# Kernel optimization log

Measured on AMD Instinct MI355X. Metric: run time of the kernel, lower is better.

Reference implementation:

```python
import jax, jax.numpy as jnp
import numpy as np

N_LAYERS = 2   # number of S6 blocks
D = 512        # input_dim / d_model
N = 16         # hid_dim (SSM state size)
O = 512        # output_dim
B = 4          # batch
L = 2048       # seq_len
LN_EPS = 1e-5


def setup_inputs() -> dict:
    key = jax.random.key(0)
    ks = jax.random.split(key, 10)
    s = D ** -0.5
    inp = {
        "x": jax.random.normal(ks[0], (B, L, D), jnp.float32),
        # per-layer S6 block params (stacked over layer axis)
        "A_log": jax.random.normal(ks[1], (N_LAYERS, D, N), jnp.float32) * 0.5,
        "W_B": jax.random.normal(ks[2], (N_LAYERS, D, N), jnp.float32) * s,
        "b_B": jnp.zeros((N_LAYERS, N), jnp.float32),
        "W_C": jax.random.normal(ks[3], (N_LAYERS, D, N), jnp.float32) * s,
        "b_C": jnp.zeros((N_LAYERS, N), jnp.float32),
        "W_dt": jax.random.normal(ks[4], (N_LAYERS, D, D), jnp.float32) * s,
        "b_dt": jnp.zeros((N_LAYERS, D), jnp.float32),
        "D_skip": jnp.ones((N_LAYERS, D), jnp.float32),
        # mixing linear + layer norm per layer
        "W_mix": jax.random.normal(ks[5], (N_LAYERS, D, D), jnp.float32) * s,
        "b_mix": jnp.zeros((N_LAYERS, D), jnp.float32),
        "ln_g": jnp.ones((N_LAYERS, D), jnp.float32),
        "ln_b": jnp.zeros((N_LAYERS, D), jnp.float32),
        # final decoder
        "W_dec": jax.random.normal(ks[6], (D, O), jnp.float32) * s,
        "b_dec": jnp.zeros((O,), jnp.float32),
    }
    return inp


def _combine(e1, e2):
    # first-order linear recurrence combine: h <- a*h + u
    a1, u1 = e1
    a2, u2 = e2
    return a1 * a2, a2 * u1 + u2


def reference(x, A_log, W_B, b_B, W_C, b_C, W_dt, b_dt, D_skip,
              W_mix, b_mix, ln_g, ln_b, W_dec, b_dec):
    h_in = x  # [B, L, D]
    for i in range(N_LAYERS):
        # ---- S6 block: input-dependent B, C, dt; diagonal A ----
        A = -jnp.exp(A_log[i])                               # [D, N], negative real
        Bm = h_in @ W_B[i] + b_B[i]                          # [B, L, N]
        Cm = h_in @ W_C[i] + b_C[i]                          # [B, L, N]
        dt = jax.nn.softplus(h_in @ W_dt[i] + b_dt[i])       # [B, L, D]
        # discretize: a_t = exp(dt*A), u_t = dt * B_t * x_t
        a = jnp.exp(dt[..., None] * A)                       # [B, L, D, N]
        u = (dt * h_in)[..., None] * Bm[:, :, None, :]       # [B, L, D, N]
        # parallel scan over sequence axis (Heinsen / Blelloch style)
        _, h = jax.lax.associative_scan(_combine, (a, u), axis=1)
        y = jnp.einsum('bln,bldn->bld', Cm, h) + D_skip[i] * h_in  # [B, L, D]
        # ---- activation (torch.nn.GELU default = exact erf) ----
        y = jax.nn.gelu(y, approximate=False)
        # ---- mixing linear ----
        y = y @ W_mix[i] + b_mix[i]
        # ---- layer norm ----
        mu = jnp.mean(y, axis=-1, keepdims=True)
        var = jnp.var(y, axis=-1, keepdims=True)
        y = (y - mu) / jnp.sqrt(var + LN_EPS) * ln_g[i] + ln_b[i]
        # ---- residual ----
        h_in = h_in + y
    return h_in @ W_dec + b_dec  # [B, L, O]
```

## Files before the change

### kernel.cpp

```cpp
#include <hip/hip_runtime.h>
#include <math.h>

typedef unsigned short u16;
typedef unsigned int u32;
typedef __attribute__((ext_vector_type(8))) short short8;
typedef __attribute__((ext_vector_type(8))) _Float16 half8;
typedef __attribute__((ext_vector_type(4))) float f32x4;

#define BL 8192
#define DD 512
#define NN 16
#define NCHUNK 64
#define SCH 32
#define ZLD 640

__device__ __forceinline__ float softplus_f(float z) {
  float w = __builtin_amdgcn_exp2f(-1.4426950408889634f * fabsf(z));
  return fmaxf(z, 0.0f) + 0.69314718055994531f * __builtin_amdgcn_logf(1.0f + w);
}

__device__ __forceinline__ float gelu_erf(float y) {
  float ax = fabsf(y) * 0.70710678118654752f;
  float t  = __builtin_amdgcn_rcpf(1.0f + 0.3275911f * ax);
  float e  = __builtin_amdgcn_exp2f(-1.4426950408889634f * ax * ax);
  float p  = ((((1.061405429f * t - 1.453152027f) * t + 1.421413741f) * t
               - 0.284496736f) * t + 0.254829592f) * t;
  float er = copysignf(1.0f - p * e, y);
  return 0.5f * y * (1.0f + er);
}

#define PREP_TOT (4194304 + 655360 + 524288 + 262144 + 1280 + 16384)
__global__ __launch_bounds__(256) void prep_kernel(
    const float* __restrict__ x, const float* __restrict__ A_log,
    const float* __restrict__ W_B, const float* __restrict__ b_B,
    const float* __restrict__ W_C, const float* __restrict__ b_C,
    const float* __restrict__ W_dt, const float* __restrict__ b_dt,
    const float* __restrict__ W_mix, const float* __restrict__ W_dec,
    _Float16* __restrict__ x16, _Float16* __restrict__ Wc16,
    _Float16* __restrict__ Wm16, _Float16* __restrict__ Wd16,
    float* __restrict__ bcat, float* __restrict__ A2)
{
  int i = blockIdx.x * 256 + threadIdx.x;
  if (i >= PREP_TOT) return;
  if (i < 4194304) { x16[i] = (_Float16)x[i]; return; }
  i -= 4194304;
  if (i < 655360) {
    int l = i / 327680, r = i % 327680, n = r >> 9, k = r & 511;
    float v = 0.0f;
    if (n < 16)       v = W_B[l * 8192 + k * 16 + n];
    else if (n < 32)  v = W_C[l * 8192 + k * 16 + (n - 16)];
    else if (n < 544) v = W_dt[l * 262144 + k * 512 + (n - 32)];
    Wc16[i] = (_Float16)v;
    return;
  }
  i -= 655360;
  if (i < 524288) {
    int l = i / 262144, r = i % 262144, n = r >> 9, k = r & 511;
    Wm16[i] = (_Float16)W_mix[l * 262144 + k * 512 + n];
    return;
  }
  i -= 524288;
  if (i < 262144) {
    int n = i >> 9, k = i & 511;
    Wd16[i] = (_Float16)W_dec[k * 512 + n];
    return;
  }
  i -= 262144;
  if (i < 1280) {
    int l = i / 640, n = i % 640;
    float v = 0.0f;
    if (n < 16)       v = b_B[l * 16 + n];
    else if (n < 32)  v = b_C[l * 16 + (n - 16)];
    else if (n < 544) v = b_dt[l * 512 + (n - 32)];
    bcat[i] = v;
    return;
  }
  i -= 1280;
  A2[i] = -expf(A_log[i]) * 1.4426950408889634f;
}

template <int MODE>
__global__ __launch_bounds__(256) void gemm_f16(
    const _Float16* __restrict__ A, const _Float16* __restrict__ Bt,
    const float* __restrict__ bias, float* __restrict__ Cmat, int ldc)
{
  const int K = 512;
  int bid = blockIdx.x;
  int xcd = bid & 7;
  int rest = bid >> 3;
  int mloc = rest & 7;
  int nb = rest >> 3;
  int m0 = (xcd * 8 + mloc) * 128;
  int n0 = nb * 64;
  __shared__ __align__(16) char smem[36864];
  _Float16* As = (_Float16*)smem;
  _Float16* Bs = As + 128 * 32;
  int tid = threadIdx.x;
  int wave = tid >> 6, lane = tid & 63;
  int wm = (wave >> 1) * 64;
  int wn = (wave & 1) * 32;
  int lrow = lane & 15;
  int lk = (lane >> 4) * 8;
  f32x4 acc[4][2] = {};

  int q0 = tid, q1 = tid + 256;
  size_t offA0 = (size_t)(m0 + (q0 >> 2)) * K + (q0 & 3) * 8;
  size_t offA1 = (size_t)(m0 + (q1 >> 2)) * K + (q1 & 3) * 8;
  size_t offB  = (size_t)(n0 + (q0 >> 2)) * K + (q0 & 3) * 8;
  unsigned l0 = (unsigned)(wave * 64) * 8;
  unsigned l1 = (unsigned)(wave * 64 + 256) * 8;

  for (int k0 = 0; k0 < K; k0 += 32) {
    __builtin_amdgcn_global_load_lds(
        (const __attribute__((address_space(1))) void*)(A + offA0 + k0),
        (__attribute__((address_space(3))) void*)(&As[l0]), 16, 0, 0);
    __builtin_amdgcn_global_load_lds(
        (const __attribute__((address_space(1))) void*)(A + offA1 + k0),
        (__attribute__((address_space(3))) void*)(&As[l1]), 16, 0, 0);
    __builtin_amdgcn_global_load_lds(
        (const __attribute__((address_space(1))) void*)(Bt + offB + k0),
        (__attribute__((address_space(3))) void*)(&Bs[l0]), 16, 0, 0);
    __syncthreads();

    half8 af[4], bf[2];
#pragma unroll
    for (int i = 0; i < 4; ++i)
      af[i] = *(const half8*)&As[(wm + i * 16 + lrow) * 32 + lk];
#pragma unroll
    for (int t = 0; t < 2; ++t)
      bf[t] = *(const half8*)&Bs[(wn + t * 16 + lrow) * 32 + lk];
#pragma unroll
    for (int i = 0; i < 4; ++i)
#pragma unroll
      for (int t = 0; t < 2; ++t)
        acc[i][t] = __builtin_amdgcn_mfma_f32_16x16x32_f16(af[i], bf[t], acc[i][t], 0, 0, 0);
    __syncthreads();
  }

  float* ct = (float*)smem + wave * (64 * 36);
  int quad = lane >> 4;
#pragma unroll
  for (int t = 0; t < 2; ++t) {
    int coll = wn + t * 16 + lrow;
    float bv = bias[n0 + coll];
    bool sp = (MODE == 1) && (n0 + coll >= 32);
#pragma unroll
    for (int i = 0; i < 4; ++i) {
#pragma unroll
      for (int r = 0; r < 4; ++r) {
        float v = acc[i][t][r] + bv;
        if (sp) v = softplus_f(v);
        ct[(i * 16 + quad * 4 + r) * 36 + (t * 16 + lrow)] = v;
      }
    }
  }
  __syncthreads();
  int r8 = lane >> 3, c8 = lane & 7;
  int colv = n0 + wn + c8 * 4;
  bool do_store = !(MODE == 1 && colv >= 544);
#pragma unroll
  for (int pass = 0; pass < 8; ++pass) {
    int rowl = pass * 8 + r8;
    float4 v = *(const float4*)&ct[rowl * 36 + c8 * 4];
    if (do_store)
      *(float4*)&Cmat[(size_t)(m0 + wm + rowl) * ldc + colv] = v;
  }
}

template <int PACKED>
__global__ __launch_bounds__(256) void scan_p1(
    const float* __restrict__ Z, const float* __restrict__ Xf,
    const _Float16* __restrict__ Xh, const float* __restrict__ A2,
    float* __restrict__ Ach, float* __restrict__ Uch)
{
  int bid = blockIdx.x;
  int dg = bid & 1, c = (bid >> 1) & (NCHUNK - 1), b = bid >> 7;
  int d = dg * 256 + threadIdx.x;
  int row0 = b * 2048 + c * SCH;
  __shared__ float Bsh[SCH * 16];
  for (int i = threadIdx.x; i < SCH * 16; i += 256)
    Bsh[i] = Z[(size_t)(row0 + (i >> 4)) * ZLD + (i & 15)];
  __syncthreads();
  float a2[16];
  const float4* a2v = (const float4*)(A2 + d * 16);
#pragma unroll
  for (int q = 0; q < 4; ++q) {
    float4 f = a2v[q];
    a2[q * 4 + 0] = f.x; a2[q * 4 + 1] = f.y; a2[q * 4 + 2] = f.z; a2[q * 4 + 3] = f.w;
  }
  float ap[16], u[16];
#pragma unroll
  for (int n = 0; n < 16; ++n) { ap[n] = 1.0f; u[n] = 0.0f; }
  for (int t = 0; t < SCH; ++t) {
    size_t row = row0 + t;
    float dtv = Z[row * ZLD + 32 + d];
    float xv = PACKED ? (float)Xh[row * DD + d] : Xf[row * DD + d];
    float dx = dtv * xv;
#pragma unroll
    for (int n = 0; n < 16; ++n) {
      float e = __builtin_amdgcn_exp2f(dtv * a2[n]);
      u[n] = e * u[n] + dx * Bsh[t * 16 + n];
      ap[n] *= e;
    }
  }
  size_t out = ((size_t)(b * NCHUNK + c) * DD + d) * 16;
#pragma unroll
  for (int n = 0; n < 16; ++n) { Ach[out + n] = ap[n]; Uch[out + n] = u[n]; }
}

__global__ __launch_bounds__(256) void scan_p2(
    const float* __restrict__ Ach, float* __restrict__ Uch)
{
  int blk = blockIdx.x;
  int b = blk >> 7;
  int dn = (blk & 127) * 64 + (threadIdx.x & 63);
  int seg = threadIdx.x >> 6;
  size_t base = (size_t)b * NCHUNK * 8192 + dn;
  float a_r[16], u_r[16];
#pragma unroll
  for (int i = 0; i < 16; ++i) {
    size_t idx = base + (size_t)(seg * 16 + i) * 8192;
    a_r[i] = Ach[idx];
    u_r[i] = Uch[idx];
  }
  float Ap = 1.0f, hA = 0.0f;
#pragma unroll
  for (int i = 0; i < 16; ++i) { hA = a_r[i] * hA + u_r[i]; Ap *= a_r[i]; }
  __shared__ float AsegL[4][64], UsegL[4][64];
  AsegL[seg][threadIdx.x & 63] = Ap;
  UsegL[seg][threadIdx.x & 63] = hA;
  __syncthreads();
  float h = 0.0f;
  for (int s = 0; s < seg; ++s)
    h = AsegL[s][threadIdx.x & 63] * h + UsegL[s][threadIdx.x & 63];
#pragma unroll
  for (int i = 0; i < 16; ++i) {
    size_t idx = base + (size_t)(seg * 16 + i) * 8192;
    Uch[idx] = h;
    h = a_r[i] * h + u_r[i];
  }
}

template <int PACKED>
__global__ __launch_bounds__(256) void scan_p3(
    const float* __restrict__ Z, const float* __restrict__ Xf,
    const _Float16* __restrict__ Xh, const float* __restrict__ A2,
    const float* __restrict__ Hinit, const float* __restrict__ Dskip,
    _Float16* __restrict__ Yout)
{
  int bid = blockIdx.x;
  int dg = bid & 1, c = (bid >> 1) & (NCHUNK - 1), b = bid >> 7;
  int d = dg * 256 + threadIdx.x;
  int row0 = b * 2048 + c * SCH;
  __shared__ float Bsh[SCH * 16];
  __shared__ float Csh[SCH * 16];
  for (int i = threadIdx.x; i < SCH * 16; i += 256) {
    size_t rz = (size_t)(row0 + (i >> 4)) * ZLD;
    Bsh[i] = Z[rz + (i & 15)];
    Csh[i] = Z[rz + 16 + (i & 15)];
  }
  __syncthreads();
  float a2[16];
  const float4* a2v = (const float4*)(A2 + d * 16);
#pragma unroll
  for (int q = 0; q < 4; ++q) {
    float4 f = a2v[q];
    a2[q * 4 + 0] = f.x; a2[q * 4 + 1] = f.y; a2[q * 4 + 2] = f.z; a2[q * 4 + 3] = f.w;
  }
  float h[16];
  size_t hidx = ((size_t)(b * NCHUNK + c) * DD + d) * 16;
#pragma unroll
  for (int n = 0; n < 16; ++n) h[n] = Hinit[hidx + n];
  float dsk = Dskip[d];
  for (int t = 0; t < SCH; ++t) {
    size_t row = row0 + t;
    float dtv = Z[row * ZLD + 32 + d];
    float xv = PACKED ? (float)Xh[row * DD + d] : Xf[row * DD + d];
    float dx = dtv * xv;
    float acc = 0.0f;
#pragma unroll
    for (int n = 0; n < 16; ++n) {
      float e = __builtin_amdgcn_exp2f(dtv * a2[n]);
      h[n] = e * h[n] + dx * Bsh[t * 16 + n];
      acc += Csh[t * 16 + n] * h[n];
    }
    float y = acc + dsk * xv;
    Yout[row * DD + d] = (_Float16)gelu_erf(y);
  }
}

template <int PACKED>
__global__ __launch_bounds__(256) void ln_residual(
    const float* __restrict__ Y2, const float* Xf,
    const float* __restrict__ gam, const float* __restrict__ bet,
    _Float16* Hh)
{
  int wave = threadIdx.x >> 6, lane = threadIdx.x & 63;
  size_t row = (size_t)blockIdx.x * 4 + wave;
  size_t gbase = row * DD + lane * 8;
  const float4* yr = (const float4*)(Y2 + gbase);
  float4 y0 = yr[0], y1 = yr[1];
  float v[8] = {y0.x, y0.y, y0.z, y0.w, y1.x, y1.y, y1.z, y1.w};
  float s = 0.0f, sq = 0.0f;
#pragma unroll
  for (int j = 0; j < 8; ++j) { s += v[j]; sq += v[j] * v[j]; }
#pragma unroll
  for (int off = 32; off; off >>= 1) {
    s += __shfl_xor(s, off, 64);
    sq += __shfl_xor(sq, off, 64);
  }
  float mu = s * (1.0f / 512.0f);
  float var = sq * (1.0f / 512.0f) - mu * mu;
  float rstd = rsqrtf(var + 1e-5f);

  float hin[8];
  if (PACKED) {
    half8 hh = *(const half8*)(Hh + gbase);
#pragma unroll
    for (int j = 0; j < 8; ++j) hin[j] = (float)hh[j];
  } else {
    const float4* xr = (const float4*)(Xf + gbase);
    float4 x0 = xr[0], x1 = xr[1];
    hin[0]=x0.x; hin[1]=x0.y; hin[2]=x0.z; hin[3]=x0.w;
    hin[4]=x1.x; hin[5]=x1.y; hin[6]=x1.z; hin[7]=x1.w;
  }
  const float4* g4 = (const float4*)(gam + lane * 8);
  const float4* b4 = (const float4*)(bet + lane * 8);
  float4 g0 = g4[0], g1 = g4[1], bb0 = b4[0], bb1 = b4[1];
  float gv[8] = {g0.x,g0.y,g0.z,g0.w,g1.x,g1.y,g1.z,g1.w};
  float bv[8] = {bb0.x,bb0.y,bb0.z,bb0.w,bb1.x,bb1.y,bb1.z,bb1.w};
  half8 sh;
#pragma unroll
  for (int j = 0; j < 8; ++j) {
    float o = (v[j] - mu) * rstd * gv[j] + bv[j] + hin[j];
    sh[j] = (_Float16)o;
  }
  *(half8*)(Hh + gbase) = sh;
}

extern "C" void kernel_launch(void* const* d_in, const int* in_sizes, int n_in,
                              void* d_out, int out_size, void* d_ws, size_t ws_size,
                              hipStream_t stream) {
  const float* x      = (const float*)d_in[0];
  const float* A_log  = (const float*)d_in[1];
  const float* W_B    = (const float*)d_in[2];
  const float* b_B    = (const float*)d_in[3];
  const float* W_C    = (const float*)d_in[4];
  const float* b_C    = (const float*)d_in[5];
  const float* W_dt   = (const float*)d_in[6];
  const float* b_dt   = (const float*)d_in[7];
  const float* D_skip = (const float*)d_in[8];
  const float* W_mix  = (const float*)d_in[9];
  const float* b_mix  = (const float*)d_in[10];
  const float* ln_g   = (const float*)d_in[11];
  const float* ln_b   = (const float*)d_in[12];
  const float* W_dec  = (const float*)d_in[13];
  const float* b_dec  = (const float*)d_in[14];

  char* ws = (char*)d_ws;
  size_t off = 0;
  _Float16* x16 = (_Float16*)(ws + off);
  float*    Ach = (float*)(ws + off);     off += 8388608;
  _Float16* y16 = (_Float16*)(ws + off);  off += 8388608;
  _Float16* h16 = (_Float16*)(ws + off);  off += 8388608;
  float* Z    = (float*)(ws + off);
  float* y2   = (float*)(ws + off); off += 20971520;
  float* Uch  = (float*)(ws + off); off += 8388608;
  _Float16* Wc16 = (_Float16*)(ws + off); off += 1310720;
  _Float16* Wm16 = (_Float16*)(ws + off); off += 1048576;
  _Float16* Wd16 = (_Float16*)(ws + off); off += 524288;
  float* bcat = (float*)(ws + off); off += 5120;
  float* A2w  = (float*)(ws + off); off += 65536;

  prep_kernel<<<(PREP_TOT + 255) / 256, 256, 0, stream>>>(
      x, A_log, W_B, b_B, W_C, b_C, W_dt, b_dt, W_mix, W_dec,
      x16, Wc16, Wm16, Wd16, bcat, A2w);

  for (int l = 0; l < 2; ++l) {
    const _Float16* Ain = (l == 0) ? x16 : h16;
    gemm_f16<1><<<576, 256, 0, stream>>>(
        Ain, Wc16 + l * 640 * 512, bcat + l * 640, Z, ZLD);
    if (l == 0) {
      scan_p1<0><<<512, 256, 0, stream>>>(Z, x, nullptr,
                                          A2w + l * 8192, Ach, Uch);
      scan_p2<<<512, 256, 0, stream>>>(Ach, Uch);
      scan_p3<0><<<512, 256, 0, stream>>>(Z, x, nullptr, A2w + l * 8192,
                                          Uch, D_skip + l * 512, y16);
    } else {
      scan_p1<1><<<512, 256, 0, stream>>>(Z, nullptr, h16,
                                          A2w + l * 8192, Ach, Uch);
      scan_p2<<<512, 256, 0, stream>>>(Ach, Uch);
      scan_p3<1><<<512, 256, 0, stream>>>(Z, nullptr, h16, A2w + l * 8192,
                                          Uch, D_skip + l * 512, y16);
    }
    gemm_f16<0><<<512, 256, 0, stream>>>(
        y16, Wm16 + l * 512 * 512, b_mix + l * 512, y2, DD);
    if (l == 0)
      ln_residual<0><<<2048, 256, 0, stream>>>(y2, x, ln_g + l * 512,
                                               ln_b + l * 512, h16);
    else
      ln_residual<1><<<2048, 256, 0, stream>>>(y2, nullptr, ln_g + l * 512,
                                               ln_b + l * 512, h16);
  }
  gemm_f16<0><<<512, 256, 0, stream>>>(
      h16, Wd16, b_dec, (float*)d_out, DD);
}
```

Before: 291.3 us.

## Fuse three scan phases into one cooperative kernel and widen GEMM K-tile with swizzle

```diff
diff --git a/kernel.cpp b/kernel.cpp
--- a/kernel.cpp
+++ b/kernel.cpp
@@ -1,9 +1,11 @@
 #include <hip/hip_runtime.h>
+#include <hip/hip_cooperative_groups.h>
 #include <math.h>
+
+namespace cg = cooperative_groups;
 
 typedef unsigned short u16;
 typedef unsigned int u32;
-typedef __attribute__((ext_vector_type(8))) short short8;
 typedef __attribute__((ext_vector_type(8))) _Float16 half8;
 typedef __attribute__((ext_vector_type(4))) float f32x4;
 
@@ -94,51 +96,58 @@
   int n0 = nb * 64;
   __shared__ __align__(16) char smem[36864];
   _Float16* As = (_Float16*)smem;
-  _Float16* Bs = As + 128 * 32;
+  _Float16* Bs = As + 128 * 64;
   int tid = threadIdx.x;
   int wave = tid >> 6, lane = tid & 63;
   int wm = (wave >> 1) * 64;
   int wn = (wave & 1) * 32;
   int lrow = lane & 15;
-  int lk = (lane >> 4) * 8;
+  int q4 = lane >> 4;
   f32x4 acc[4][2] = {};
 
-  int q0 = tid, q1 = tid + 256;
-  size_t offA0 = (size_t)(m0 + (q0 >> 2)) * K + (q0 & 3) * 8;
-  size_t offA1 = (size_t)(m0 + (q1 >> 2)) * K + (q1 & 3) * 8;
-  size_t offB  = (size_t)(n0 + (q0 >> 2)) * K + (q0 & 3) * 8;
-  unsigned l0 = (unsigned)(wave * 64) * 8;
-  unsigned l1 = (unsigned)(wave * 64 + 256) * 8;
-
-  for (int k0 = 0; k0 < K; k0 += 32) {
-    __builtin_amdgcn_global_load_lds(
-        (const __attribute__((address_space(1))) void*)(A + offA0 + k0),
-        (__attribute__((address_space(3))) void*)(&As[l0]), 16, 0, 0);
-    __builtin_amdgcn_global_load_lds(
-        (const __attribute__((address_space(1))) void*)(A + offA1 + k0),
-        (__attribute__((address_space(3))) void*)(&As[l1]), 16, 0, 0);
-    __builtin_amdgcn_global_load_lds(
-        (const __attribute__((address_space(1))) void*)(Bt + offB + k0),
-        (__attribute__((address_space(3))) void*)(&Bs[l0]), 16, 0, 0);
+  int srow = tid >> 3;
+  int scol = ((tid & 7) ^ (srow & 7)) * 8;
+  size_t gA = (size_t)(m0 + srow) * K + scol;
+  size_t gB = (size_t)(n0 + srow) * K + scol;
+  unsigned sdst = (unsigned)(wave * 512);
+
+  for (int k0 = 0; k0 < K; k0 += 64) {
+#pragma unroll
+    for (int j = 0; j < 4; ++j)
+      __builtin_amdgcn_global_load_lds(
+          (const __attribute__((address_space(1))) void*)(A + gA + (size_t)(j * 32) * K + k0),
+          (__attribute__((address_space(3))) void*)(&As[j * 2048 + sdst]), 16, 0, 0);
+#pragma unroll
+    for (int j = 0; j < 2; ++j)
+      __builtin_amdgcn_global_load_lds(
+          (const __attribute__((address_space(1))) void*)(Bt + gB + (size_t)(j * 32) * K + k0),
+          (__attribute__((address_space(3))) void*)(&Bs[j * 2048 + sdst]), 16, 0, 0);
     __syncthreads();
-
-    half8 af[4], bf[2];
-#pragma unroll
-    for (int i = 0; i < 4; ++i)
-      af[i] = *(const half8*)&As[(wm + i * 16 + lrow) * 32 + lk];
-#pragma unroll
-    for (int t = 0; t < 2; ++t)
-      bf[t] = *(const half8*)&Bs[(wn + t * 16 + lrow) * 32 + lk];
-#pragma unroll
-    for (int i = 0; i < 4; ++i)
-#pragma unroll
-      for (int t = 0; t < 2; ++t)
-        acc[i][t] = __builtin_amdgcn_mfma_f32_16x16x32_f16(af[i], bf[t], acc[i][t], 0, 0, 0);
+#pragma unroll
+    for (int kk = 0; kk < 2; ++kk) {
+      half8 af[4], bf[2];
+#pragma unroll
+      for (int i = 0; i < 4; ++i) {
+        int r = wm + i * 16 + lrow;
+        int cb = (kk * 4 + q4) ^ (lrow & 7);
+        af[i] = *(const half8*)&As[r * 64 + cb * 8];
+      }
+#pragma unroll
+      for (int t = 0; t < 2; ++t) {
+        int r = wn + t * 16 + lrow;
+        int cb = (kk * 4 + q4) ^ (lrow & 7);
+        bf[t] = *(const half8*)&Bs[r * 64 + cb * 8];
+      }
+#pragma unroll
+      for (int i = 0; i < 4; ++i)
+#pragma unroll
+        for (int t = 0; t < 2; ++t)
+          acc[i][t] = __builtin_amdgcn_mfma_f32_16x16x32_f16(af[i], bf[t], acc[i][t], 0, 0, 0);
+    }
     __syncthreads();
   }
 
   float* ct = (float*)smem + wave * (64 * 36);
-  int quad = lane >> 4;
 #pragma unroll
   for (int t = 0; t < 2; ++t) {
     int coll = wn + t * 16 + lrow;
@@ -150,7 +159,7 @@
       for (int r = 0; r < 4; ++r) {
         float v = acc[i][t][r] + bv;
         if (sp) v = softplus_f(v);
-        ct[(i * 16 + quad * 4 + r) * 36 + (t * 16 + lrow)] = v;
+        ct[(i * 16 + q4 * 4 + r) * 36 + (t * 16 + lrow)] = v;
       }
     }
   }
@@ -168,92 +177,20 @@
 }
 
 template <int PACKED>
-__global__ __launch_bounds__(256) void scan_p1(
+__global__ __launch_bounds__(256, 2) void scan_fused(
     const float* __restrict__ Z, const float* __restrict__ Xf,
     const _Float16* __restrict__ Xh, const float* __restrict__ A2,
-    float* __restrict__ Ach, float* __restrict__ Uch)
+    float* __restrict__ Ach, float* __restrict__ Uch,
+    const float* __restrict__ Dskip, _Float16* __restrict__ Yout)
 {
-  int bid = blockIdx.x;
-  int dg = bid & 1, c = (bid >> 1) & (NCHUNK - 1), b = bid >> 7;
-  int d = dg * 256 + threadIdx.x;
-  int row0 = b * 2048 + c * SCH;
-  __shared__ float Bsh[SCH * 16];
-  for (int i = threadIdx.x; i < SCH * 16; i += 256)
-    Bsh[i] = Z[(size_t)(row0 + (i >> 4)) * ZLD + (i & 15)];
-  __syncthreads();
-  float a2[16];
-  const float4* a2v = (const float4*)(A2 + d * 16);
-#pragma unroll
-  for (int q = 0; q < 4; ++q) {
-    float4 f = a2v[q];
-    a2[q * 4 + 0] = f.x; a2[q * 4 + 1] = f.y; a2[q * 4 + 2] = f.z; a2[q * 4 + 3] = f.w;
-  }
-  float ap[16], u[16];
-#pragma unroll
-  for (int n = 0; n < 16; ++n) { ap[n] = 1.0f; u[n] = 0.0f; }
-  for (int t = 0; t < SCH; ++t) {
-    size_t row = row0 + t;
-    float dtv = Z[row * ZLD + 32 + d];
-    float xv = PACKED ? (float)Xh[row * DD + d] : Xf[row * DD + d];
-    float dx = dtv * xv;
-#pragma unroll
-    for (int n = 0; n < 16; ++n) {
-      float e = __builtin_amdgcn_exp2f(dtv * a2[n]);
-      u[n] = e * u[n] + dx * Bsh[t * 16 + n];
-      ap[n] *= e;
-    }
-  }
-  size_t out = ((size_t)(b * NCHUNK + c) * DD + d) * 16;
-#pragma unroll
-  for (int n = 0; n < 16; ++n) { Ach[out + n] = ap[n]; Uch[out + n] = u[n]; }
-}
-
-__global__ __launch_bounds__(256) void scan_p2(
-    const float* __restrict__ Ach, float* __restrict__ Uch)
-{
-  int blk = blockIdx.x;
-  int b = blk >> 7;
-  int dn = (blk & 127) * 64 + (threadIdx.x & 63);
-  int seg = threadIdx.x >> 6;
-  size_t base = (size_t)b * NCHUNK * 8192 + dn;
-  float a_r[16], u_r[16];
-#pragma unroll
-  for (int i = 0; i < 16; ++i) {
-    size_t idx = base + (size_t)(seg * 16 + i) * 8192;
-    a_r[i] = Ach[idx];
-    u_r[i] = Uch[idx];
-  }
-  float Ap = 1.0f, hA = 0.0f;
-#pragma unroll
-  for (int i = 0; i < 16; ++i) { hA = a_r[i] * hA + u_r[i]; Ap *= a_r[i]; }
-  __shared__ float AsegL[4][64], UsegL[4][64];
-  AsegL[seg][threadIdx.x & 63] = Ap;
-  UsegL[seg][threadIdx.x & 63] = hA;
-  __syncthreads();
-  float h = 0.0f;
-  for (int s = 0; s < seg; ++s)
-    h = AsegL[s][threadIdx.x & 63] * h + UsegL[s][threadIdx.x & 63];
-#pragma unroll
-  for (int i = 0; i < 16; ++i) {
-    size_t idx = base + (size_t)(seg * 16 + i) * 8192;
-    Uch[idx] = h;
-    h = a_r[i] * h + u_r[i];
-  }
-}
-
-template <int PACKED>
-__global__ __launch_bounds__(256) void scan_p3(
-    const float* __restrict__ Z, const float* __restrict__ Xf,
-    const _Float16* __restrict__ Xh, const float* __restrict__ A2,
-    const float* __restrict__ Hinit, const float* __restrict__ Dskip,
-    _Float16* __restrict__ Yout)
-{
+  cg::grid_group grid = cg::this_grid();
   int bid = blockIdx.x;
   int dg = bid & 1, c = (bid >> 1) & (NCHUNK - 1), b = bid >> 7;
   int d = dg * 256 + threadIdx.x;
   int row0 = b * 2048 + c * SCH;
   __shared__ float Bsh[SCH * 16];
   __shared__ float Csh[SCH * 16];
+  __shared__ float AsegL[4][64], UsegL[4][64];
   for (int i = threadIdx.x; i < SCH * 16; i += 256) {
     size_t rz = (size_t)(row0 + (i >> 4)) * ZLD;
     Bsh[i] = Z[rz + (i & 15)];
@@ -267,25 +204,82 @@
     float4 f = a2v[q];
     a2[q * 4 + 0] = f.x; a2[q * 4 + 1] = f.y; a2[q * 4 + 2] = f.z; a2[q * 4 + 3] = f.w;
   }
-  float h[16];
-  size_t hidx = ((size_t)(b * NCHUNK + c) * DD + d) * 16;
-#pragma unroll
-  for (int n = 0; n < 16; ++n) h[n] = Hinit[hidx + n];
-  float dsk = Dskip[d];
-  for (int t = 0; t < SCH; ++t) {
-    size_t row = row0 + t;
-    float dtv = Z[row * ZLD + 32 + d];
-    float xv = PACKED ? (float)Xh[row * DD + d] : Xf[row * DD + d];
-    float dx = dtv * xv;
-    float acc = 0.0f;
-#pragma unroll
-    for (int n = 0; n < 16; ++n) {
-      float e = __builtin_amdgcn_exp2f(dtv * a2[n]);
-      h[n] = e * h[n] + dx * Bsh[t * 16 + n];
-      acc += Csh[t * 16 + n] * h[n];
-    }
-    float y = acc + dsk * xv;
-    Yout[row * DD + d] = (_Float16)gelu_erf(y);
+
+  {
+    float ap[16], u[16];
+#pragma unroll
+    for (int n = 0; n < 16; ++n) { ap[n] = 1.0f; u[n] = 0.0f; }
+    for (int t = 0; t < SCH; ++t) {
+      size_t row = row0 + t;
+      float dtv = Z[row * ZLD + 32 + d];
+      float xv = PACKED ? (float)Xh[row * DD + d] : Xf[row * DD + d];
+      float dx = dtv * xv;
+#pragma unroll
+      for (int n = 0; n < 16; ++n) {
+        float e = __builtin_amdgcn_exp2f(dtv * a2[n]);
+        u[n] = e * u[n] + dx * Bsh[t * 16 + n];
+        ap[n] *= e;
+      }
+    }
+    size_t out = ((size_t)(b * NCHUNK + c) * DD + d) * 16;
+#pragma unroll
+    for (int n = 0; n < 16; ++n) { Ach[out + n] = ap[n]; Uch[out + n] = u[n]; }
+  }
+  __threadfence();
+  grid.sync();
+
+  {
+    int b2 = bid >> 7;
+    int dn = (bid & 127) * 64 + (threadIdx.x & 63);
+    int seg = threadIdx.x >> 6;
+    size_t base = (size_t)b2 * NCHUNK * 8192 + dn;
+    float a_r[16], u_r[16];
+#pragma unroll
+    for (int i = 0; i < 16; ++i) {
+      size_t idx = base + (size_t)(seg * 16 + i) * 8192;
+      a_r[i] = Ach[idx];
+      u_r[i] = Uch[idx];
+    }
+    float Ap = 1.0f, hA = 0.0f;
+#pragma unroll
+    for (int i = 0; i < 16; ++i) { hA = a_r[i] * hA + u_r[i]; Ap *= a_r[i]; }
+    AsegL[seg][threadIdx.x & 63] = Ap;
+    UsegL[seg][threadIdx.x & 63] = hA;
+    __syncthreads();
+    float h = 0.0f;
+    for (int s = 0; s < seg; ++s)
+      h = AsegL[s][threadIdx.x & 63] * h + UsegL[s][threadIdx.x & 63];
+#pragma unroll
+    for (int i = 0; i < 16; ++i) {
+      size_t idx = base + (size_t)(seg * 16 + i) * 8192;
+      Uch[idx] = h;
+      h = a_r[i] * h + u_r[i];
+    }
+  }
+  __threadfence();
+  grid.sync();
+
+  {
+    float h[16];
+    size_t hidx = ((size_t)(b * NCHUNK + c) * DD + d) * 16;
+#pragma unroll
+    for (int n = 0; n < 16; ++n) h[n] = Uch[hidx + n];
+    float dsk = Dskip[d];
+    for (int t = 0; t < SCH; ++t) {
+      size_t row = row0 + t;
+      float dtv = Z[row * ZLD + 32 + d];
+      float xv = PACKED ? (float)Xh[row * DD + d] : Xf[row * DD + d];
+      float dx = dtv * xv;
+      float acc = 0.0f;
+#pragma unroll
+      for (int n = 0; n < 16; ++n) {
+        float e = __builtin_amdgcn_exp2f(dtv * a2[n]);
+        h[n] = e * h[n] + dx * Bsh[t * 16 + n];
+        acc += Csh[t * 16 + n] * h[n];
+      }
+      float y = acc + dsk * xv;
+      Yout[row * DD + d] = (_Float16)gelu_erf(y);
+    }
   }
 }
 
@@ -380,19 +374,27 @@
     const _Float16* Ain = (l == 0) ? x16 : h16;
     gemm_f16<1><<<576, 256, 0, stream>>>(
         Ain, Wc16 + l * 640 * 512, bcat + l * 640, Z, ZLD);
-    if (l == 0) {
-      scan_p1<0><<<512, 256, 0, stream>>>(Z, x, nullptr,
-                                          A2w + l * 8192, Ach, Uch);
-      scan_p2<<<512, 256, 0, stream>>>(Ach, Uch);
-      scan_p3<0><<<512, 256, 0, stream>>>(Z, x, nullptr, A2w + l * 8192,
-                                          Uch, D_skip + l * 512, y16);
-    } else {
-      scan_p1<1><<<512, 256, 0, stream>>>(Z, nullptr, h16,
-                                          A2w + l * 8192, Ach, Uch);
-      scan_p2<<<512, 256, 0, stream>>>(Ach, Uch);
-      scan_p3<1><<<512, 256, 0, stream>>>(Z, nullptr, h16, A2w + l * 8192,
-                                          Uch, D_skip + l * 512, y16);
-    }
+
+    {
+      const float* Zc = Z;
+      const float* Xfc = (l == 0) ? x : nullptr;
+      const _Float16* Xhc = (l == 0) ? nullptr : h16;
+      const float* A2c = A2w + l * 8192;
+      float* Achc = Ach; float* Uchc = Uch;
+      const float* Dc = D_skip + l * 512;
+      _Float16* Yc = y16;
+      void* args[] = {&Zc, &Xfc, &Xhc, &A2c, &Achc, &Uchc, &Dc, &Yc};
+      if (l == 0) {
+        void (*fn)(const float*, const float*, const _Float16*, const float*,
+                   float*, float*, const float*, _Float16*) = scan_fused<0>;
+        hipLaunchCooperativeKernel((void*)fn, dim3(512), dim3(256), args, 0, stream);
+      } else {
+        void (*fn)(const float*, const float*, const _Float16*, const float*,
+                   float*, float*, const float*, _Float16*) = scan_fused<1>;
+        hipLaunchCooperativeKernel((void*)fn, dim3(512), dim3(256), args, 0, stream);
+      }
+    }
+
     gemm_f16<0><<<512, 256, 0, stream>>>(
         y16, Wm16 + l * 512 * 512, b_mix + l * 512, y2, DD);
     if (l == 0)
```

New measurement: 759.5 us. +160.7%, slower.
